# Optimization experiments

Hardware: AMD Instinct MI355X
Metric: run time of the kernel (lower is better)

## Reference

```python
import jax, jax.numpy as jnp
import numpy as np

N_NODES = 50000
TAU = 1.0 + (1.0 / 1000.0) * (0.1 - 1.0)  # anneal step 1 -> 0.9991


def setup_inputs() -> dict:
    key = jax.random.key(0)
    ks = jax.random.split(key, 8)
    N, F, H, E, K = N_NODES, 128, 128, 800000, 5
    node_features = jax.random.normal(ks[0], (N, F), dtype=jnp.float32)
    src = jnp.sort(jax.random.randint(ks[1], (E,), 0, N, dtype=jnp.int32))
    dst = jax.random.randint(ks[2], (E,), 0, N, dtype=jnp.int32)
    u_noise = jax.random.uniform(ks[3], (K, E), dtype=jnp.float32,
                                 minval=1e-6, maxval=1.0 - 1e-6)
    # MLP params: Linear(2F -> H), ReLU, Linear(H -> 1)
    W1 = jax.random.normal(ks[4], (2 * F, H), dtype=jnp.float32) / np.sqrt(2 * F)
    b1 = jnp.zeros((H,), dtype=jnp.float32)
    W2 = jax.random.normal(ks[5], (H, 1), dtype=jnp.float32) / np.sqrt(H)
    b2 = jnp.zeros((1,), dtype=jnp.float32)
    return {"node_features": node_features, "W1": W1, "b1": b1,
            "W2": W2, "b2": b2, "u_noise": u_noise, "src": src, "dst": dst}


def reference(node_features, W1, b1, W2, b2, u_noise, src, dst):
    N = N_NODES
    F = node_features.shape[1]
    # per-edge MLP on concat([x_u, x_v]) without materializing the (E, 2F) concat
    x_u = node_features[src]                      # (E, F)
    x_v = node_features[dst]                      # (E, F)
    h = jax.nn.relu(x_u @ W1[:F] + x_v @ W1[F:] + b1)   # (E, H)
    z = (h @ W2 + b2)[:, 0]                       # (E,)
    # per-node (segment) log-softmax over each node's neighbor edges
    zmax = jax.ops.segment_max(z, src, num_segments=N)
    ze = z - zmax[src]
    denom = jax.ops.segment_sum(jnp.exp(ze), src, num_segments=N)
    log_pi = ze - jnp.log(denom)[src]             # (E,)
    # k rounds of Gumbel-softmax sampling
    g = -jnp.log(-jnp.log(u_noise))               # (K, E)
    scores = (log_pi[None, :] + g) / TAU          # (K, E)

    def seg_softmax(s):
        m = jax.ops.segment_max(s, src, num_segments=N)
        e = jnp.exp(s - m[src])
        return e / jax.ops.segment_sum(e, src, num_segments=N)[src]

    def seg_argmax_dst(s):
        m = jax.ops.segment_max(s, src, num_segments=N)
        hit = s >= m[src]
        sel = jax.ops.segment_max(jnp.where(hit, dst, -1), src, num_segments=N)
        return sel  # (N,) selected neighbor per node, per round

    soft = jax.vmap(seg_softmax)(scores)          # (K, E) gumbel-softmax probs
    selected = jax.vmap(seg_argmax_dst)(scores)   # (K, N) sampled neighbor ids
    return selected, soft
```

## Files before the change

kernel.cpp:

```cpp
#include <hip/hip_runtime.h>

#define FEAT 128
#define HID  128
#define XS_S 132
#define MAXE 2048

__global__ __launch_bounds__(256) void gemm_ab(
    const float* __restrict__ X, const float* __restrict__ W1,
    const float* __restrict__ b1, float* __restrict__ A,
    float* __restrict__ B, int N) {
  __shared__ float xs[32 * XS_S];
  __shared__ float ws[32 * 64];
  const int t = threadIdx.x;

  const int nbk = gridDim.x;
  const int q = nbk >> 3, r = nbk & 7;
  const int xcd = blockIdx.x & 7, bidx = blockIdx.x >> 3;
  const int nw = (xcd < r ? xcd * (q + 1) : r * (q + 1) + (xcd - r) * q) + bidx;
  const int n0 = (nw >> 2) * 128;
  const int j0 = (nw & 3) * 64;
  const bool isA = j0 < 128;
  const float* Wbase = W1 + (isA ? j0 : 128 * HID + (j0 - 128));
  float* Obase = isA ? (A + j0) : (B + (j0 - 128));

  const int tn = t & 31;
  const int tc = t >> 5;

  float acc[4][8];
#pragma unroll
  for (int rr = 0; rr < 4; ++rr)
#pragma unroll
    for (int c = 0; c < 8; ++c) acc[rr][c] = 0.f;

  const int ln = t >> 3;
  const int lf = (t & 7) * 4;

  for (int kc = 0; kc < 4; ++kc) {
    __syncthreads();
#pragma unroll
    for (int rep = 0; rep < 4; ++rep) {
      const int nl = ln + rep * 32;
      const int n = n0 + nl;
      float4 v = make_float4(0.f, 0.f, 0.f, 0.f);
      if (n < N) v = *(const float4*)(X + (size_t)n * FEAT + kc * 32 + lf);
      xs[(lf + 0) * XS_S + nl] = v.x;
      xs[(lf + 1) * XS_S + nl] = v.y;
      xs[(lf + 2) * XS_S + nl] = v.z;
      xs[(lf + 3) * XS_S + nl] = v.w;
    }
#pragma unroll
    for (int rep = 0; rep < 2; ++rep) {
      const int idx = rep * 256 + t;
      const int wr = idx >> 4;
      const int c4 = (idx & 15) * 4;
      *(float4*)&ws[wr * 64 + c4] =
          *(const float4*)(Wbase + (size_t)(kc * 32 + wr) * HID + c4);
    }
    __syncthreads();

#pragma unroll 8
    for (int k = 0; k < 32; ++k) {
      const float4 xv = *(const float4*)&xs[k * XS_S + tn * 4];
      const float4 w0 = *(const float4*)&ws[k * 64 + tc * 8];
      const float4 w1 = *(const float4*)&ws[k * 64 + tc * 8 + 4];
      const float xr[4] = {xv.x, xv.y, xv.z, xv.w};
#pragma unroll
      for (int rr = 0; rr < 4; ++rr) {
        acc[rr][0] = fmaf(xr[rr], w0.x, acc[rr][0]);
        acc[rr][1] = fmaf(xr[rr], w0.y, acc[rr][1]);
        acc[rr][2] = fmaf(xr[rr], w0.z, acc[rr][2]);
        acc[rr][3] = fmaf(xr[rr], w0.w, acc[rr][3]);
        acc[rr][4] = fmaf(xr[rr], w1.x, acc[rr][4]);
        acc[rr][5] = fmaf(xr[rr], w1.y, acc[rr][5]);
        acc[rr][6] = fmaf(xr[rr], w1.z, acc[rr][6]);
        acc[rr][7] = fmaf(xr[rr], w1.w, acc[rr][7]);
      }
    }
  }

  float bb[8];
#pragma unroll
  for (int c = 0; c < 8; ++c) bb[c] = 0.f;
  if (isA) {
    *(float4*)&bb[0] = *(const float4*)(b1 + j0 + tc * 8);
    *(float4*)&bb[4] = *(const float4*)(b1 + j0 + tc * 8 + 4);
  }
#pragma unroll
  for (int rr = 0; rr < 4; ++rr) {
    const int n = n0 + tn * 4 + rr;
    if (n < N) {
      float* o = Obase + (size_t)n * HID + tc * 8;
      *(float4*)o = make_float4(acc[rr][0] + bb[0], acc[rr][1] + bb[1],
                                acc[rr][2] + bb[2], acc[rr][3] + bb[3]);
      *(float4*)(o + 4) = make_float4(acc[rr][4] + bb[4], acc[rr][5] + bb[5],
                                      acc[rr][6] + bb[6], acc[rr][7] + bb[7]);
    }
  }
}

__global__ __launch_bounds__(256) void fused_edge_seg(
    const float* __restrict__ A, const float* __restrict__ B,
    const float* __restrict__ W2, const float* __restrict__ b2,
    const int* __restrict__ src, const int* __restrict__ dst,
    const float* __restrict__ U, float* __restrict__ out_sel,
    float* __restrict__ out_soft, int N, int E, int K) {
  __shared__ float zs[MAXE];
  __shared__ int srcs[MAXE];
  __shared__ int dsts[MAXE];
  __shared__ int rsl[17];
  const int t = threadIdx.x;
  const int n0 = blockIdx.x * 16;
  const float INVTAU = 1.0f / 0.9991f;

  if (t < 17) {
    const int n = min(n0 + t, N);
    int lo = 0, hi = E;
    while (lo < hi) {
      const int mid = (lo + hi) >> 1;
      if (src[mid] < n) lo = mid + 1; else hi = mid;
    }
    rsl[t] = lo;
  }
  __syncthreads();
  const int e_lo = rsl[0];
  const int cnt = min(rsl[16] - e_lo, MAXE);

  for (int i = t; i < cnt; i += 256) {
    srcs[i] = src[e_lo + i];
    dsts[i] = dst[e_lo + i];
  }
  __syncthreads();

  {
    const int g = t >> 4;
    const int l = t & 15;
    const float4 w0 = *(const float4*)(W2 + l * 8);
    const float4 w1 = *(const float4*)(W2 + l * 8 + 4);
    const float bias2 = b2[0];
    for (int base = 0; base < cnt; base += 32) {
      const int i0 = base + g * 2;
      if (i0 < cnt) {
        const int i1 = i0 + 1;
        const bool has1 = i1 < cnt;
        const int u0 = srcs[i0], v0 = dsts[i0];
        const int u1 = has1 ? srcs[i1] : u0;
        const int v1 = has1 ? dsts[i1] : v0;

        const float4* Au0 = (const float4*)(A + (size_t)u0 * HID) + l * 2;
        const float4* Bv0 = (const float4*)(B + (size_t)v0 * HID) + l * 2;
        const float4* Au1 = (const float4*)(A + (size_t)u1 * HID) + l * 2;
        const float4* Bv1 = (const float4*)(B + (size_t)v1 * HID) + l * 2;

        const float4 a00 = Au0[0], a01 = Au0[1];
        const float4 b00 = Bv0[0], b01 = Bv0[1];
        const float4 a10 = Au1[0], a11 = Au1[1];
        const float4 b10 = Bv1[0], b11 = Bv1[1];

        float p0 = fmaxf(a00.x + b00.x, 0.f) * w0.x
                 + fmaxf(a00.y + b00.y, 0.f) * w0.y
                 + fmaxf(a00.z + b00.z, 0.f) * w0.z
                 + fmaxf(a00.w + b00.w, 0.f) * w0.w
                 + fmaxf(a01.x + b01.x, 0.f) * w1.x
                 + fmaxf(a01.y + b01.y, 0.f) * w1.y
                 + fmaxf(a01.z + b01.z, 0.f) * w1.z
                 + fmaxf(a01.w + b01.w, 0.f) * w1.w;
        float p1 = fmaxf(a10.x + b10.x, 0.f) * w0.x
                 + fmaxf(a10.y + b10.y, 0.f) * w0.y
                 + fmaxf(a10.z + b10.z, 0.f) * w0.z
                 + fmaxf(a10.w + b10.w, 0.f) * w0.w
                 + fmaxf(a11.x + b11.x, 0.f) * w1.x
                 + fmaxf(a11.y + b11.y, 0.f) * w1.y
                 + fmaxf(a11.z + b11.z, 0.f) * w1.z
                 + fmaxf(a11.w + b11.w, 0.f) * w1.w;

#pragma unroll
        for (int m = 8; m >= 1; m >>= 1) {
          p0 += __shfl_xor(p0, m);
          p1 += __shfl_xor(p1, m);
        }
        if (l == 0) {
          zs[i0] = p0 + bias2;
          if (has1) zs[i1] = p1 + bias2;
        }
      }
    }
  }
  __syncthreads();

  const int lane = t & 63;
  const int qtr = lane >> 4;
  const int ql = lane & 15;
  const int li = (t >> 6) * 4 + qtr;
  const int n = n0 + li;

  int start = 0, deg = 0;
  if (n < N) { start = rsl[li]; deg = rsl[li + 1] - start; }

  if (__all(deg <= 32)) {
    if (n >= N) return;
    if (deg == 0) {
      if (ql == 0)
        for (int k = 0; k < K; ++k) out_sel[(size_t)k * N + n] = -2147483648.0f;
      return;
    }
    const bool a0 = 2 * ql < deg;
    const bool a1 = 2 * ql + 1 < deg;
    const int le0 = start - e_lo + 2 * ql;
    const int le1 = le0 + 1;
    const int e0 = start + 2 * ql;
    const int e1 = e0 + 1;
    const float z0 = a0 ? zs[le0] : -INFINITY;
    const float z1 = a1 ? zs[le1] : -INFINITY;
    const int d0 = a0 ? dsts[le0] : -1;
    const int d1 = a1 ? dsts[le1] : -1;

    float zmax = fmaxf(z0, z1);
#pragma unroll
    for (int m = 8; m >= 1; m >>= 1) zmax = fmaxf(zmax, __shfl_xor(zmax, m));
    float den = (a0 ? __expf(z0 - zmax) : 0.f) + (a1 ? __expf(z1 - zmax) : 0.f);
#pragma unroll
    for (int m = 8; m >= 1; m >>= 1) den += __shfl_xor(den, m);
    const float logd = __logf(den);
    const float lp0 = (z0 - zmax) - logd;
    const float lp1 = (z1 - zmax) - logd;

    for (int k = 0; k < K; ++k) {
      float ex0 = 0.f, ex1 = 0.f;
      if (a0) {
        const float uu = U[(size_t)k * E + e0];
        const float gum = -__logf(-__logf(uu));
        ex0 = __expf((lp0 + gum) * INVTAU);
      }
      if (a1) {
        const float uu = U[(size_t)k * E + e1];
        const float gum = -__logf(-__logf(uu));
        ex1 = __expf((lp1 + gum) * INVTAU);
      }
      float d2 = ex0 + ex1;
      float mx;
      int md;
      if (ex1 > ex0)      { mx = ex1; md = d1; }
      else if (ex1 < ex0) { mx = ex0; md = d0; }
      else                { mx = ex0; md = max(d0, d1); }
#pragma unroll
      for (int m = 8; m >= 1; m >>= 1) {
        d2 += __shfl_xor(d2, m);
        const float ox = __shfl_xor(mx, m);
        const int od = __shfl_xor(md, m);
        if (ox > mx) { mx = ox; md = od; }
        else if (ox == mx) md = max(md, od);
      }
      if (ql == 0) out_sel[(size_t)k * N + n] = (float)md;
      const float inv = __builtin_amdgcn_rcpf(d2);
      if (a0) out_soft[(size_t)k * E + e0] = ex0 * inv;
      if (a1) out_soft[(size_t)k * E + e1] = ex1 * inv;
    }
    return;
  }

  const int lbase = (t >> 6) * 4;
  for (int j = 0; j < 4; ++j) {
    const int lj = lbase + j;
    const int nn = n0 + lj;
    if (nn >= N) continue;
    const int st = rsl[lj];
    const int dg = rsl[lj + 1] - st;
    const int lst = st - e_lo;
    if (dg == 0) {
      if (lane == 0)
        for (int k = 0; k < K; ++k) out_sel[(size_t)k * N + nn] = -2147483648.0f;
      continue;
    }
    float zmax = -INFINITY;
    for (int c = lane; c < dg; c += 64) zmax = fmaxf(zmax, zs[lst + c]);
#pragma unroll
    for (int m = 32; m >= 1; m >>= 1) zmax = fmaxf(zmax, __shfl_xor(zmax, m));
    float den = 0.f;
    for (int c = lane; c < dg; c += 64) den += expf(zs[lst + c] - zmax);
#pragma unroll
    for (int m = 32; m >= 1; m >>= 1) den += __shfl_xor(den, m);
    const float logd = logf(den);

    for (int k = 0; k < K; ++k) {
      float m2 = -INFINITY;
      for (int c = lane; c < dg; c += 64) {
        const float gum = -logf(-logf(U[(size_t)k * E + st + c]));
        const float s = ((zs[lst + c] - zmax) - logd + gum) * INVTAU;
        m2 = fmaxf(m2, s);
      }
#pragma unroll
      for (int m = 32; m >= 1; m >>= 1) m2 = fmaxf(m2, __shfl_xor(m2, m));
      float d2 = 0.f;
      int cand = -1;
      for (int c = lane; c < dg; c += 64) {
        const float gum = -logf(-logf(U[(size_t)k * E + st + c]));
        const float s = ((zs[lst + c] - zmax) - logd + gum) * INVTAU;
        d2 += expf(s - m2);
        if (s >= m2) cand = max(cand, dsts[lst + c]);
      }
#pragma unroll
      for (int m = 32; m >= 1; m >>= 1) d2 += __shfl_xor(d2, m);
#pragma unroll
      for (int m = 32; m >= 1; m >>= 1) cand = max(cand, __shfl_xor(cand, m));
      if (lane == 0) out_sel[(size_t)k * N + nn] = (float)cand;
      for (int c = lane; c < dg; c += 64) {
        const float gum = -logf(-logf(U[(size_t)k * E + st + c]));
        const float s = ((zs[lst + c] - zmax) - logd + gum) * INVTAU;
        out_soft[(size_t)k * E + st + c] = expf(s - m2) / d2;
      }
    }
  }
}

extern "C" void kernel_launch(void* const* d_in, const int* in_sizes, int n_in,
                              void* d_out, int out_size, void* d_ws, size_t ws_size,
                              hipStream_t stream) {
  const float* X  = (const float*)d_in[0];
  const float* W1 = (const float*)d_in[1];
  const float* b1 = (const float*)d_in[2];
  const float* W2 = (const float*)d_in[3];
  const float* b2 = (const float*)d_in[4];
  const float* U  = (const float*)d_in[5];
  const int* src  = (const int*)d_in[6];
  const int* dst  = (const int*)d_in[7];
  const int E = in_sizes[6];
  const int K = in_sizes[5] / E;
  const int N = in_sizes[0] / FEAT;

  float* A = (float*)d_ws;
  float* B = A + (size_t)N * HID;

  float* out_sel  = (float*)d_out;
  float* out_soft = (float*)d_out + (size_t)K * N;

  hipLaunchKernelGGL(gemm_ab, dim3(4 * ((N + 127) / 128)), dim3(256), 0, stream,
                     X, W1, b1, A, B, N);
  hipLaunchKernelGGL(fused_edge_seg, dim3((N + 15) / 16), dim3(256), 0, stream,
                     A, B, W2, b2, src, dst, U, out_sel, out_soft, N, E, K);
}
```

Before: 238.0 us.

## Split fused edge kernel into separate edge-score and segment-sampling kernels

```diff
diff --git a/kernel.cpp b/kernel.cpp
--- a/kernel.cpp
+++ b/kernel.cpp
@@ -3,7 +3,6 @@
 #define FEAT 128
 #define HID  128
 #define XS_S 132
-#define MAXE 2048
 
 __global__ __launch_bounds__(256) void gemm_ab(
     const float* __restrict__ X, const float* __restrict__ W1,
@@ -98,92 +97,82 @@
   }
 }
 
-__global__ __launch_bounds__(256) void fused_edge_seg(
+__global__ __launch_bounds__(256) void edge_z(
     const float* __restrict__ A, const float* __restrict__ B,
     const float* __restrict__ W2, const float* __restrict__ b2,
     const int* __restrict__ src, const int* __restrict__ dst,
-    const float* __restrict__ U, float* __restrict__ out_sel,
-    float* __restrict__ out_soft, int N, int E, int K) {
-  __shared__ float zs[MAXE];
-  __shared__ int srcs[MAXE];
-  __shared__ int dsts[MAXE];
+    float* __restrict__ z, int E) {
+  const int g = threadIdx.x >> 4;
+  const int l = threadIdx.x & 15;
+  const int e0 = blockIdx.x * 32 + g * 2;
+  if (e0 >= E) return;
+  const int e1 = e0 + 1;
+  const bool has1 = e1 < E;
+
+  const int u0 = src[e0], v0 = dst[e0];
+  const int u1 = has1 ? src[e1] : u0;
+  const int v1 = has1 ? dst[e1] : v0;
+
+  const float4* Au0 = (const float4*)(A + (size_t)u0 * HID) + l * 2;
+  const float4* Bv0 = (const float4*)(B + (size_t)v0 * HID) + l * 2;
+  const float4* Au1 = (const float4*)(A + (size_t)u1 * HID) + l * 2;
+  const float4* Bv1 = (const float4*)(B + (size_t)v1 * HID) + l * 2;
+
+  const float4 a00 = Au0[0], a01 = Au0[1];
+  const float4 b00 = Bv0[0], b01 = Bv0[1];
+  const float4 a10 = Au1[0], a11 = Au1[1];
+  const float4 b10 = Bv1[0], b11 = Bv1[1];
+
+  const float4 w0 = *(const float4*)(W2 + l * 8);
+  const float4 w1 = *(const float4*)(W2 + l * 8 + 4);
+  const float bias2 = b2[0];
+
+  float p0 = fmaxf(a00.x + b00.x, 0.f) * w0.x
+           + fmaxf(a00.y + b00.y, 0.f) * w0.y
+           + fmaxf(a00.z + b00.z, 0.f) * w0.z
+           + fmaxf(a00.w + b00.w, 0.f) * w0.w
+           + fmaxf(a01.x + b01.x, 0.f) * w1.x
+           + fmaxf(a01.y + b01.y, 0.f) * w1.y
+           + fmaxf(a01.z + b01.z, 0.f) * w1.z
+           + fmaxf(a01.w + b01.w, 0.f) * w1.w;
+  float p1 = fmaxf(a10.x + b10.x, 0.f) * w0.x
+           + fmaxf(a10.y + b10.y, 0.f) * w0.y
+           + fmaxf(a10.z + b10.z, 0.f) * w0.z
+           + fmaxf(a10.w + b10.w, 0.f) * w0.w
+           + fmaxf(a11.x + b11.x, 0.f) * w1.x
+           + fmaxf(a11.y + b11.y, 0.f) * w1.y
+           + fmaxf(a11.z + b11.z, 0.f) * w1.z
+           + fmaxf(a11.w + b11.w, 0.f) * w1.w;
+
+#pragma unroll
+  for (int m = 8; m >= 1; m >>= 1) {
+    p0 += __shfl_xor(p0, m);
+    p1 += __shfl_xor(p1, m);
+  }
+  if (l == 0) {
+    z[e0] = p0 + bias2;
+    if (has1) z[e1] = p1 + bias2;
+  }
+}
+
+__global__ __launch_bounds__(256) void seg_sample(
+    const float* __restrict__ z, const float* __restrict__ U,
+    const int* __restrict__ src, const int* __restrict__ dst,
+    float* __restrict__ out_sel, float* __restrict__ out_soft,
+    int N, int E, int K) {
   __shared__ int rsl[17];
   const int t = threadIdx.x;
   const int n0 = blockIdx.x * 16;
   const float INVTAU = 1.0f / 0.9991f;
 
   if (t < 17) {
-    const int n = min(n0 + t, N);
+    const int nn = min(n0 + t, N);
     int lo = 0, hi = E;
     while (lo < hi) {
       const int mid = (lo + hi) >> 1;
-      if (src[mid] < n) lo = mid + 1; else hi = mid;
+      if (src[mid] < nn) lo = mid + 1; else hi = mid;
     }
     rsl[t] = lo;
-  }
-  __syncthreads();
-  const int e_lo = rsl[0];
-  const int cnt = min(rsl[16] - e_lo, MAXE);
-
-  for (int i = t; i < cnt; i += 256) {
-    srcs[i] = src[e_lo + i];
-    dsts[i] = dst[e_lo + i];
-  }
-  __syncthreads();
-
-  {
-    const int g = t >> 4;
-    const int l = t & 15;
-    const float4 w0 = *(const float4*)(W2 + l * 8);
-    const float4 w1 = *(const float4*)(W2 + l * 8 + 4);
-    const float bias2 = b2[0];
-    for (int base = 0; base < cnt; base += 32) {
-      const int i0 = base + g * 2;
-      if (i0 < cnt) {
-        const int i1 = i0 + 1;
-        const bool has1 = i1 < cnt;
-        const int u0 = srcs[i0], v0 = dsts[i0];
-        const int u1 = has1 ? srcs[i1] : u0;
-        const int v1 = has1 ? dsts[i1] : v0;
-
-        const float4* Au0 = (const float4*)(A + (size_t)u0 * HID) + l * 2;
-        const float4* Bv0 = (const float4*)(B + (size_t)v0 * HID) + l * 2;
-        const float4* Au1 = (const float4*)(A + (size_t)u1 * HID) + l * 2;
-        const float4* Bv1 = (const float4*)(B + (size_t)v1 * HID) + l * 2;
-
-        const float4 a00 = Au0[0], a01 = Au0[1];
-        const float4 b00 = Bv0[0], b01 = Bv0[1];
-        const float4 a10 = Au1[0], a11 = Au1[1];
-        const float4 b10 = Bv1[0], b11 = Bv1[1];
-
-        float p0 = fmaxf(a00.x + b00.x, 0.f) * w0.x
-                 + fmaxf(a00.y + b00.y, 0.f) * w0.y
-                 + fmaxf(a00.z + b00.z, 0.f) * w0.z
-                 + fmaxf(a00.w + b00.w, 0.f) * w0.w
-                 + fmaxf(a01.x + b01.x, 0.f) * w1.x
-                 + fmaxf(a01.y + b01.y, 0.f) * w1.y
-                 + fmaxf(a01.z + b01.z, 0.f) * w1.z
-                 + fmaxf(a01.w + b01.w, 0.f) * w1.w;
-        float p1 = fmaxf(a10.x + b10.x, 0.f) * w0.x
-                 + fmaxf(a10.y + b10.y, 0.f) * w0.y
-                 + fmaxf(a10.z + b10.z, 0.f) * w0.z
-                 + fmaxf(a10.w + b10.w, 0.f) * w0.w
-                 + fmaxf(a11.x + b11.x, 0.f) * w1.x
-                 + fmaxf(a11.y + b11.y, 0.f) * w1.y
-                 + fmaxf(a11.z + b11.z, 0.f) * w1.z
-                 + fmaxf(a11.w + b11.w, 0.f) * w1.w;
-
-#pragma unroll
-        for (int m = 8; m >= 1; m >>= 1) {
-          p0 += __shfl_xor(p0, m);
-          p1 += __shfl_xor(p1, m);
-        }
-        if (l == 0) {
-          zs[i0] = p0 + bias2;
-          if (has1) zs[i1] = p1 + bias2;
-        }
-      }
-    }
   }
   __syncthreads();
 
@@ -205,14 +194,12 @@
     }
     const bool a0 = 2 * ql < deg;
     const bool a1 = 2 * ql + 1 < deg;
-    const int le0 = start - e_lo + 2 * ql;
-    const int le1 = le0 + 1;
     const int e0 = start + 2 * ql;
     const int e1 = e0 + 1;
-    const float z0 = a0 ? zs[le0] : -INFINITY;
-    const float z1 = a1 ? zs[le1] : -INFINITY;
-    const int d0 = a0 ? dsts[le0] : -1;
-    const int d1 = a1 ? dsts[le1] : -1;
+    const float z0 = a0 ? z[e0] : -INFINITY;
+    const float z1 = a1 ? z[e1] : -INFINITY;
+    const int d0 = a0 ? dst[e0] : -1;
+    const int d1 = a1 ? dst[e1] : -1;
 
     float zmax = fmaxf(z0, z1);
 #pragma unroll
@@ -265,18 +252,17 @@
     if (nn >= N) continue;
     const int st = rsl[lj];
     const int dg = rsl[lj + 1] - st;
-    const int lst = st - e_lo;
     if (dg == 0) {
       if (lane == 0)
         for (int k = 0; k < K; ++k) out_sel[(size_t)k * N + nn] = -2147483648.0f;
       continue;
     }
     float zmax = -INFINITY;
-    for (int c = lane; c < dg; c += 64) zmax = fmaxf(zmax, zs[lst + c]);
+    for (int c = lane; c < dg; c += 64) zmax = fmaxf(zmax, z[st + c]);
 #pragma unroll
     for (int m = 32; m >= 1; m >>= 1) zmax = fmaxf(zmax, __shfl_xor(zmax, m));
     float den = 0.f;
-    for (int c = lane; c < dg; c += 64) den += expf(zs[lst + c] - zmax);
+    for (int c = lane; c < dg; c += 64) den += expf(z[st + c] - zmax);
 #pragma unroll
     for (int m = 32; m >= 1; m >>= 1) den += __shfl_xor(den, m);
     const float logd = logf(den);
@@ -284,8 +270,9 @@
     for (int k = 0; k < K; ++k) {
       float m2 = -INFINITY;
       for (int c = lane; c < dg; c += 64) {
-        const float gum = -logf(-logf(U[(size_t)k * E + st + c]));
-        const float s = ((zs[lst + c] - zmax) - logd + gum) * INVTAU;
+        const int e = st + c;
+        const float gum = -logf(-logf(U[(size_t)k * E + e]));
+        const float s = ((z[e] - zmax) - logd + gum) * INVTAU;
         m2 = fmaxf(m2, s);
       }
 #pragma unroll
@@ -293,10 +280,11 @@
       float d2 = 0.f;
       int cand = -1;
       for (int c = lane; c < dg; c += 64) {
-        const float gum = -logf(-logf(U[(size_t)k * E + st + c]));
-        const float s = ((zs[lst + c] - zmax) - logd + gum) * INVTAU;
+        const int e = st + c;
+        const float gum = -logf(-logf(U[(size_t)k * E + e]));
+        const float s = ((z[e] - zmax) - logd + gum) * INVTAU;
         d2 += expf(s - m2);
-        if (s >= m2) cand = max(cand, dsts[lst + c]);
+        if (s >= m2) cand = max(cand, dst[e]);
       }
 #pragma unroll
       for (int m = 32; m >= 1; m >>= 1) d2 += __shfl_xor(d2, m);
@@ -304,9 +292,10 @@
       for (int m = 32; m >= 1; m >>= 1) cand = max(cand, __shfl_xor(cand, m));
       if (lane == 0) out_sel[(size_t)k * N + nn] = (float)cand;
       for (int c = lane; c < dg; c += 64) {
-        const float gum = -logf(-logf(U[(size_t)k * E + st + c]));
-        const float s = ((zs[lst + c] - zmax) - logd + gum) * INVTAU;
-        out_soft[(size_t)k * E + st + c] = expf(s - m2) / d2;
+        const int e = st + c;
+        const float gum = -logf(-logf(U[(size_t)k * E + e]));
+        const float s = ((z[e] - zmax) - logd + gum) * INVTAU;
+        out_soft[(size_t)k * E + e] = expf(s - m2) / d2;
       }
     }
   }
@@ -329,12 +318,15 @@
 
   float* A = (float*)d_ws;
   float* B = A + (size_t)N * HID;
+  float* z = B + (size_t)N * HID;
 
   float* out_sel  = (float*)d_out;
   float* out_soft = (float*)d_out + (size_t)K * N;
 
   hipLaunchKernelGGL(gemm_ab, dim3(4 * ((N + 127) / 128)), dim3(256), 0, stream,
                      X, W1, b1, A, B, N);
-  hipLaunchKernelGGL(fused_edge_seg, dim3((N + 15) / 16), dim3(256), 0, stream,
-                     A, B, W2, b2, src, dst, U, out_sel, out_soft, N, E, K);
+  hipLaunchKernelGGL(edge_z, dim3((E + 31) / 32), dim3(256), 0, stream,
+                     A, B, W2, b2, src, dst, z, E);
+  hipLaunchKernelGGL(seg_sample, dim3((N + 15) / 16), dim3(256), 0, stream,
+                     z, U, src, dst, out_sel, out_soft, N, E, K);
 }
```

After: 250.7 us. 1.05x slower.
